# Optimization experiments

Measured on AMD Instinct MI355X. Metric: run time of the kernel, lower is better.

The kernel has to match this reference:

```python
import jax, jax.numpy as jnp
import numpy as np

B, L, H = 2, 1024, 768
DI, N, K, R = 1536, 16, 4, 48


def setup_inputs() -> dict:
    key = jax.random.key(0)
    ks = jax.random.split(key, 10)
    s = 0.02
    inp = {
        "x": jax.random.normal(ks[0], (B, L, H), jnp.float32),
        "in_up_w": jax.random.normal(ks[1], (2 * DI * 4, H), jnp.float32) * s,
        "in_down_w": jax.random.normal(ks[2], (2 * DI, 2 * DI * 4), jnp.float32) * s,
        "conv_w": jax.random.normal(ks[3], (DI, 1, K), jnp.float32) * 0.5,
        "conv_b": jnp.zeros((DI,), jnp.float32),
        "x_proj_w": jax.random.normal(ks[4], (R + 2 * N, DI), jnp.float32) * s,
        "dt_w": jax.random.normal(ks[5], (DI, R), jnp.float32) * s,
        "dt_b": jnp.full((DI,), -4.0, jnp.float32) + jax.random.normal(ks[6], (DI,), jnp.float32) * 0.1,
        "A_log": jnp.log(jnp.broadcast_to(jnp.arange(1, N + 1, dtype=jnp.float32)[None, :], (DI, N))),
        "D": jnp.ones((DI,), jnp.float32),
        "out_up_w": jax.random.normal(ks[7], (4 * DI, DI), jnp.float32) * s,
        "out_down_w": jax.random.normal(ks[8], (H, 4 * DI), jnp.float32) * s,
    }
    return inp


def reference(x, in_up_w, in_down_w, conv_w, conv_b, x_proj_w, dt_w, dt_b,
              A_log, D, out_up_w, out_down_w):
    act = jax.nn.silu
    # in_up_proj -> act -> in_down_proj  (use_bias=False)
    proj = act(x @ in_up_w.T) @ in_down_w.T          # [B, L, 2*DI]
    proj = proj.transpose(0, 2, 1)                   # [B, 2*DI, L]
    hs, gate = jnp.split(proj, 2, axis=1)            # each [B, DI, L]

    # depthwise causal conv1d (pad left K-1, truncate to L) + SiLU
    k = conv_w.shape[-1]
    c = hs.shape[1]
    y = jax.lax.conv_general_dilated(
        hs, conv_w, window_strides=(1,), padding=[(k - 1, 0)],
        feature_group_count=c, dimension_numbers=("NCH", "OIH", "NCH"))
    hs = act(y + conv_b[None, :, None])              # [B, DI, L]

    # x_proj -> split into dt / B / C
    ssm_p = jnp.einsum("bdl,kd->blk", hs, x_proj_w)  # [B, L, R+2N]
    r = dt_w.shape[1]
    n = A_log.shape[1]
    ts, Bm, Cm = jnp.split(ssm_p, [r, r + n], axis=-1)
    dt = jax.nn.softplus(ts @ dt_w.T + dt_b)         # [B, L, DI]
    dt = dt.transpose(0, 2, 1)                       # [B, DI, L]

    A = -jnp.exp(A_log)                              # [DI, N]
    dA = jnp.exp(dt[..., None] * A[None, :, None, :])        # [B, DI, L, N]
    dBu = dt[..., None] * Bm[:, None, :, :] * hs[..., None]  # [B, DI, L, N]

    def step(s, inps):
        dA_t, dBu_t, C_t = inps          # [B,DI,N], [B,DI,N], [B,N]
        s = dA_t * s + dBu_t
        return s, jnp.einsum("bdn,bn->bd", s, C_t)

    s0 = jnp.zeros((x.shape[0], c, n), x.dtype)
    _, ys = jax.lax.scan(
        step, s0,
        (dA.transpose(2, 0, 1, 3), dBu.transpose(2, 0, 1, 3), Cm.transpose(1, 0, 2)))
    yscan = ys.transpose(1, 2, 0)                    # [B, DI, L]

    yscan = yscan + hs * D[None, :, None]
    yscan = yscan * act(gate)

    # out_up_proj -> act -> out_down_proj (use_bias=False)
    out = act(yscan.transpose(0, 2, 1) @ out_up_w.T) @ out_down_w.T  # [B, L, H]
    return out
```

## Files before the change

### kernel.cpp

```cpp
#include <hip/hip_runtime.h>
#include <hip/hip_bf16.h>
#include <cstdint>

#define B_   2
#define L_   1024
#define H_   768
#define DI_  1536
#define DI2_ 3072
#define DUP_ 12288
#define DOUT_ 6144
#define N_   16
#define R_   48
#define SPW  128
#define BL_  2048
#define C_   64
#define CL_  16

typedef __bf16 bf16x8 __attribute__((ext_vector_type(8)));
typedef float  f32x4  __attribute__((ext_vector_type(4)));
typedef unsigned int u32;

__device__ __forceinline__ float silu_f(float v) {
    return v / (1.f + __expf(-v));
}

__device__ __forceinline__ void async_ld16(const void* g, void* lds) {
    __builtin_amdgcn_global_load_lds(
        (const __attribute__((address_space(1))) u32*)g,
        (__attribute__((address_space(3))) u32*)lds, 16, 0, 0);
}

__global__ void cvt_bf16(const float* __restrict__ src, __bf16* __restrict__ dst, int n)
{
    const int i = (blockIdx.x * blockDim.x + threadIdx.x) * 8;
    if (i < n) {
        const float4 a = *(const float4*)(src + i);
        const float4 b = *(const float4*)(src + i + 4);
        bf16x8 v;
        v[0] = (__bf16)a.x; v[1] = (__bf16)a.y; v[2] = (__bf16)a.z; v[3] = (__bf16)a.w;
        v[4] = (__bf16)b.x; v[5] = (__bf16)b.y; v[6] = (__bf16)b.z; v[7] = (__bf16)b.w;
        *(bf16x8*)(dst + i) = v;
    }
}

__global__ void pad_xp(const float* __restrict__ xp, __bf16* __restrict__ dst)
{
    const int i = (blockIdx.x * blockDim.x + threadIdx.x) * 8;
    const int j = i / DI_;
    bf16x8 v;
    if (j < 80) {
        const float4 a = *(const float4*)(xp + i);
        const float4 b = *(const float4*)(xp + i + 4);
        v[0] = (__bf16)a.x; v[1] = (__bf16)a.y; v[2] = (__bf16)a.z; v[3] = (__bf16)a.w;
        v[4] = (__bf16)b.x; v[5] = (__bf16)b.y; v[6] = (__bf16)b.z; v[7] = (__bf16)b.w;
    } else {
        for (int k = 0; k < 8; ++k) v[k] = (__bf16)0.f;
    }
    *(bf16x8*)(dst + i) = v;
}

__global__ void transpose_dtw(const float* __restrict__ w, float* __restrict__ wT)
{
    const int i = blockIdx.x * blockDim.x + threadIdx.x;
    const int r = i / DI_, d = i % DI_;
    wT[i] = w[(size_t)d * R_ + r];
}

template<int EPI, int ATOMIC, typename OutT>
__global__ __launch_bounds__(256) void gemm_bf16(
    const __bf16* __restrict__ A, const __bf16* __restrict__ W, OutT* __restrict__ O,
    int M, int N, int Kslice, int lda, int ldw, int ldo)
{
    constexpr int BM = 128, BN = 128, BK = 32;
    __shared__ __bf16 As[BM * BK];
    __shared__ __bf16 Bs[BN * BK];

    const int tid  = threadIdx.x;
    const int bm   = blockIdx.x * BM;
    const int bn   = blockIdx.y * BN;
    const int kbase = blockIdx.z * Kslice;

    const int wave = tid >> 6, lane = tid & 63;
    const int wm = (wave >> 1) * 64, wn = (wave & 1) * 64;
    const int quad = lane >> 4, tr = lane & 15;

    const int srow = tid >> 2;
    const int skc  = ((tid & 3) ^ ((srow >> 1) & 3)) * 8;
    const __bf16* Ag0 = A + (size_t)(bm + srow) * lda + kbase + skc;
    const __bf16* Ag1 = A + (size_t)(bm + srow + 64) * lda + kbase + skc;
    const __bf16* Wg0 = W + (size_t)(bn + srow) * ldw + kbase + skc;
    const __bf16* Wg1 = W + (size_t)(bn + srow + 64) * ldw + kbase + skc;
    __bf16* Al0 = &As[tid * 8];
    __bf16* Al1 = &As[2048 + tid * 8];
    __bf16* Bl0 = &Bs[tid * 8];
    __bf16* Bl1 = &Bs[2048 + tid * 8];

    const int fsw = (quad ^ ((tr >> 1) & 3)) * 8;
    const __bf16* arp = &As[(wm + tr) * BK + fsw];
    const __bf16* brp = &Bs[(wn + tr) * BK + fsw];

    f32x4 acc[4][4];
#pragma unroll
    for (int i = 0; i < 4; ++i)
#pragma unroll
        for (int j = 0; j < 4; ++j) acc[i][j] = (f32x4){0.f, 0.f, 0.f, 0.f};

    for (int k0 = 0; k0 < Kslice; k0 += BK) {
        __syncthreads();
        async_ld16(Ag0 + k0, Al0);
        async_ld16(Ag1 + k0, Al1);
        async_ld16(Wg0 + k0, Bl0);
        async_ld16(Wg1 + k0, Bl1);
        __syncthreads();

        bf16x8 af[4], bfv[4];
#pragma unroll
        for (int i = 0; i < 4; ++i) af[i]  = *(const bf16x8*)(arp + i * 16 * BK);
#pragma unroll
        for (int j = 0; j < 4; ++j) bfv[j] = *(const bf16x8*)(brp + j * 16 * BK);
#pragma unroll
        for (int i = 0; i < 4; ++i)
#pragma unroll
            for (int j = 0; j < 4; ++j)
                acc[i][j] = __builtin_amdgcn_mfma_f32_16x16x32_bf16(af[i], bfv[j], acc[i][j], 0, 0, 0);
    }

#pragma unroll
    for (int i = 0; i < 4; ++i) {
        const int row = bm + wm + i * 16 + quad * 4;
#pragma unroll
        for (int j = 0; j < 4; ++j) {
            const int col = bn + wn + j * 16 + tr;
            OutT* op = O + (size_t)row * ldo + col;
#pragma unroll
            for (int r = 0; r < 4; ++r) {
                float v = acc[i][j][r];
                if (EPI == 1) v = silu_f(v);
                if (ATOMIC == 1) atomicAdd((float*)(op + (size_t)r * ldo), v);
                else             op[(size_t)r * ldo] = (OutT)v;
            }
        }
    }
}

__global__ void conv_kernel(const float* __restrict__ P,
                            const float* __restrict__ cw, const float* __restrict__ cb,
                            float* __restrict__ HS, __bf16* __restrict__ HSb)
{
    const int t = blockIdx.x * blockDim.x + threadIdx.x;
    const int d = t % DI_;
    const int bl = t / DI_;
    const int l = bl % L_;
    const float4 w = *(const float4*)(cw + (size_t)d * 4);
    const float wk[4] = {w.x, w.y, w.z, w.w};
    float acc = cb[d];
#pragma unroll
    for (int k = 0; k < 4; ++k) {
        const int ls = l - 3 + k;
        if (ls >= 0)
            acc += wk[k] * P[(size_t)(bl - l + ls) * DI2_ + d];
    }
    const float h = silu_f(acc);
    HS[t]  = h;
    HSb[t] = (__bf16)h;
}

__global__ void dt_kernel(const float* __restrict__ SP, const float* __restrict__ dtwT,
                          const float* __restrict__ dtb, float* __restrict__ DT)
{
    const int t = blockIdx.x * blockDim.x + threadIdx.x;
    const int d = t % DI_;
    const int bl = t / DI_;
    const float* ts = SP + (size_t)bl * SPW;
    float s = dtb[d];
#pragma unroll
    for (int r4 = 0; r4 < R_ / 4; ++r4) {
        const float4 tv = *(const float4*)(ts + r4 * 4);
        const float* wp = dtwT + (size_t)r4 * 4 * DI_ + d;
        s += tv.x * wp[0] + tv.y * wp[DI_] + tv.z * wp[2 * DI_] + tv.w * wp[3 * DI_];
    }
    DT[t] = (s > 20.f) ? s : log1pf(__expf(s));
}

__global__ __launch_bounds__(256) void scan_pass1(
    const float* __restrict__ DT, const float* __restrict__ HS,
    const float* __restrict__ SP, const float* __restrict__ A_log,
    float* __restrict__ Aprod, float* __restrict__ Bacc)
{
    const int t = blockIdx.x * blockDim.x + threadIdx.x;
    const int d = t % DI_;
    const int y = t / DI_;
    const int c = y % C_;
    const int b = y / C_;
    float A[N_], s[N_], ap[N_];
    {
        const float4* alp = (const float4*)(A_log + (size_t)d * N_);
        const float4 a0 = alp[0], a1 = alp[1], a2 = alp[2], a3 = alp[3];
        const float av[N_] = {a0.x,a0.y,a0.z,a0.w, a1.x,a1.y,a1.z,a1.w,
                              a2.x,a2.y,a2.z,a2.w, a3.x,a3.y,a3.z,a3.w};
#pragma unroll
        for (int n = 0; n < N_; ++n) { A[n] = -__expf(av[n]); s[n] = 0.f; ap[n] = 1.f; }
    }
    for (int il = 0; il < CL_; ++il) {
        const size_t bl = (size_t)b * L_ + c * CL_ + il;
        const float dt = DT[bl * DI_ + d];
        const float hs = HS[bl * DI_ + d];
        const float4* Bp = (const float4*)(SP + bl * SPW + R_);
        const float4 b0 = Bp[0], b1 = Bp[1], b2 = Bp[2], b3 = Bp[3];
        const float Bv[N_] = {b0.x,b0.y,b0.z,b0.w, b1.x,b1.y,b1.z,b1.w,
                              b2.x,b2.y,b2.z,b2.w, b3.x,b3.y,b3.z,b3.w};
        const float dh = dt * hs;
#pragma unroll
        for (int n = 0; n < N_; ++n) {
            const float dA = __expf(dt * A[n]);
            s[n] = fmaf(dA, s[n], dh * Bv[n]);
            ap[n] *= dA;
        }
    }
    float4* Ap = (float4*)(Aprod + (size_t)t * N_);
    float4* Bc = (float4*)(Bacc  + (size_t)t * N_);
    Ap[0] = make_float4(ap[0], ap[1], ap[2], ap[3]);
    Ap[1] = make_float4(ap[4], ap[5], ap[6], ap[7]);
    Ap[2] = make_float4(ap[8], ap[9], ap[10], ap[11]);
    Ap[3] = make_float4(ap[12], ap[13], ap[14], ap[15]);
    Bc[0] = make_float4(s[0], s[1], s[2], s[3]);
    Bc[1] = make_float4(s[4], s[5], s[6], s[7]);
    Bc[2] = make_float4(s[8], s[9], s[10], s[11]);
    Bc[3] = make_float4(s[12], s[13], s[14], s[15]);
}

__global__ __launch_bounds__(256) void scan_pass2(
    const float* __restrict__ Aprod, const float* __restrict__ Bacc,
    float* __restrict__ Sinit)
{
    const int t = blockIdx.x * blockDim.x + threadIdx.x;
    const int n = t & (N_ - 1);
    const int d = (t >> 4) % DI_;
    const int b = (t >> 4) / DI_;
    float s = 0.f;
    for (int c = 0; c < C_; ++c) {
        const size_t idx = (((size_t)b * C_ + c) * DI_ + d) * N_ + n;
        Sinit[idx] = s;
        s = fmaf(Aprod[idx], s, Bacc[idx]);
    }
}

__global__ __launch_bounds__(256) void scan_pass3(
    const float* __restrict__ DT, const float* __restrict__ HS,
    const float* __restrict__ SP, const float* __restrict__ P,
    const float* __restrict__ A_log, const float* __restrict__ Dv,
    const float* __restrict__ Sinit, __bf16* __restrict__ Y)
{
    const int t = blockIdx.x * blockDim.x + threadIdx.x;
    const int d = t % DI_;
    const int y = t / DI_;
    const int c = y % C_;
    const int b = y / C_;
    float A[N_], s[N_];
    {
        const float4* alp = (const float4*)(A_log + (size_t)d * N_);
        const float4 a0 = alp[0], a1 = alp[1], a2 = alp[2], a3 = alp[3];
        const float av[N_] = {a0.x,a0.y,a0.z,a0.w, a1.x,a1.y,a1.z,a1.w,
                              a2.x,a2.y,a2.z,a2.w, a3.x,a3.y,a3.z,a3.w};
#pragma unroll
        for (int n = 0; n < N_; ++n) A[n] = -__expf(av[n]);
    }
    {
        const float4* sp = (const float4*)(Sinit + (size_t)t * N_);
        const float4 s0 = sp[0], s1 = sp[1], s2 = sp[2], s3 = sp[3];
        s[0]=s0.x; s[1]=s0.y; s[2]=s0.z; s[3]=s0.w;
        s[4]=s1.x; s[5]=s1.y; s[6]=s1.z; s[7]=s1.w;
        s[8]=s2.x; s[9]=s2.y; s[10]=s2.z; s[11]=s2.w;
        s[12]=s3.x; s[13]=s3.y; s[14]=s3.z; s[15]=s3.w;
    }
    const float Dd = Dv[d];
    for (int il = 0; il < CL_; ++il) {
        const size_t bl = (size_t)b * L_ + c * CL_ + il;
        const float dt = DT[bl * DI_ + d];
        const float hs = HS[bl * DI_ + d];
        const float4* Bp = (const float4*)(SP + bl * SPW + R_);
        const float4 b0 = Bp[0], b1 = Bp[1], b2 = Bp[2], b3 = Bp[3];
        const float4 c0 = Bp[4], c1 = Bp[5], c2 = Bp[6], c3 = Bp[7];
        const float Bv[N_] = {b0.x,b0.y,b0.z,b0.w, b1.x,b1.y,b1.z,b1.w,
                              b2.x,b2.y,b2.z,b2.w, b3.x,b3.y,b3.z,b3.w};
        const float Cv[N_] = {c0.x,c0.y,c0.z,c0.w, c1.x,c1.y,c1.z,c1.w,
                              c2.x,c2.y,c2.z,c2.w, c3.x,c3.y,c3.z,c3.w};
        const float dh = dt * hs;
        float acc = 0.f;
#pragma unroll
        for (int n = 0; n < N_; ++n) {
            const float dA = __expf(dt * A[n]);
            s[n] = fmaf(dA, s[n], dh * Bv[n]);
            acc = fmaf(s[n], Cv[n], acc);
        }
        const float g = P[bl * DI2_ + DI_ + d];
        Y[bl * DI_ + d] = (__bf16)((acc + hs * Dd) * silu_f(g));
    }
}

extern "C" void kernel_launch(void* const* d_in, const int* in_sizes, int n_in,
                              void* d_out, int out_size, void* d_ws, size_t ws_size,
                              hipStream_t stream) {
    const float* x        = (const float*)d_in[0];
    const float* w_up     = (const float*)d_in[1];
    const float* w_down   = (const float*)d_in[2];
    const float* conv_w   = (const float*)d_in[3];
    const float* conv_b   = (const float*)d_in[4];
    const float* x_proj_w = (const float*)d_in[5];
    const float* dt_w     = (const float*)d_in[6];
    const float* dt_b     = (const float*)d_in[7];
    const float* A_log    = (const float*)d_in[8];
    const float* Dvec     = (const float*)d_in[9];
    const float* w_oup    = (const float*)d_in[10];
    const float* w_odown  = (const float*)d_in[11];
    float* out = (float*)d_out;

    char* base = (char*)d_ws;
    __bf16* x_b      = (__bf16*)base;
    __bf16* wup_b    = (__bf16*)(base + 3145728);
    float*  P        = (float*)base;
    char* r2 = base + 25165824;
    __bf16* wdown_b  = (__bf16*)r2;
    __bf16* HSb      = (__bf16*)r2;
    float*  SPb      = (float*)(r2 + 6291456);
    float*  DTb      = (float*)(r2 + 7340032);
    __bf16* Yb       = (__bf16*)(r2 + 19922944);
    __bf16* XPpad    = (__bf16*)(r2 + 26214400);
    float*  dtwT     = (float*)(r2 + 26607616);
    __bf16* woup_b   = (__bf16*)(r2 + 26902528);
    __bf16* wodown_b = (__bf16*)(r2 + 45776896);
    char* r3 = r2 + 75497472;
    __bf16* U1b      = (__bf16*)r3;
    __bf16* U2b      = (__bf16*)r3;
    float*  Aprod    = (float*)r3;
    float*  Bacc     = (float*)(r3 + 12582912);
    float*  Sinit    = (float*)(r3 + 25165824);
    char* r4 = r3 + 50331648;
    float*  HS       = (float*)r4;

    cvt_bf16<<<(BL_ * H_) / 2048, 256, 0, stream>>>(x, x_b, BL_ * H_);
    cvt_bf16<<<(DUP_ * H_) / 2048, 256, 0, stream>>>(w_up, wup_b, DUP_ * H_);
    cvt_bf16<<<(DI2_ * DUP_) / 2048, 256, 0, stream>>>(w_down, wdown_b, DI2_ * DUP_);

    gemm_bf16<1, 0, __bf16><<<dim3(16, 96, 1), 256, 0, stream>>>(
        x_b, wup_b, U1b, BL_, DUP_, H_, H_, H_, DUP_);

    hipMemsetAsync(P, 0, (size_t)BL_ * DI2_ * 4, stream);
    gemm_bf16<0, 1, float><<<dim3(16, 24, 4), 256, 0, stream>>>(
        U1b, wdown_b, P, BL_, DI2_, DUP_ / 4, DUP_, DUP_, DI2_);

    pad_xp<<<(128 * DI_) / 2048, 256, 0, stream>>>(x_proj_w, XPpad);
    transpose_dtw<<<(R_ * DI_) / 256, 256, 0, stream>>>(dt_w, dtwT);
    cvt_bf16<<<(DOUT_ * DI_) / 2048, 256, 0, stream>>>(w_oup, woup_b, DOUT_ * DI_);
    cvt_bf16<<<(H_ * DOUT_) / 2048, 256, 0, stream>>>(w_odown, wodown_b, H_ * DOUT_);

    conv_kernel<<<(BL_ * DI_) / 256, 256, 0, stream>>>(P, conv_w, conv_b, HS, HSb);

    hipMemsetAsync(SPb, 0, (size_t)BL_ * SPW * 4, stream);
    gemm_bf16<0, 1, float><<<dim3(16, 1, 4), 256, 0, stream>>>(
        HSb, XPpad, SPb, BL_, SPW, DI_ / 4, DI_, DI_, SPW);

    dt_kernel<<<(BL_ * DI_) / 256, 256, 0, stream>>>(SPb, dtwT, dt_b, DTb);

    scan_pass1<<<(B_ * C_ * DI_) / 256, 256, 0, stream>>>(DTb, HS, SPb, A_log, Aprod, Bacc);
    scan_pass2<<<(B_ * DI_ * N_) / 256, 256, 0, stream>>>(Aprod, Bacc, Sinit);
    scan_pass3<<<(B_ * C_ * DI_) / 256, 256, 0, stream>>>(
        DTb, HS, SPb, P, A_log, Dvec, Sinit, Yb);

    gemm_bf16<1, 0, __bf16><<<dim3(16, 48, 1), 256, 0, stream>>>(
        Yb, woup_b, U2b, BL_, DOUT_, DI_, DI_, DI_, DOUT_);

    hipMemsetAsync(out, 0, (size_t)BL_ * H_ * 4, stream);
    gemm_bf16<0, 1, float><<<dim3(16, 6, 8), 256, 0, stream>>>(
        U2b, wodown_b, out, BL_, H_, DOUT_ / 8, DOUT_, DOUT_, H_);
}
```

Measured before the change: 856.5 us.

## Add 256x256-tile 512-thread GEMM with 4-stage async pipeline for two projections

Introduces a new GEMM kernel with 256x256 output tiles, 8 waves, a 4-slot LDS ring filled by async global-to-LDS loads, XOR-swizzled shared layout, split A/B staging interleaved with MFMA phases, s_setprio around the MFMA blocks, and a grouped block-index swizzle for L2 locality. It replaces the in_down split-K GEMM (now split 8 ways) and the out_up GEMM. The larger tiles raise arithmetic intensity and cut global/LDS traffic per FLOP. In exchange it uses 128 KB of dynamic LDS and many accumulator registers, which limits occupancy, and the grids become much smaller, which risks underfilling the CUs.

```diff
diff --git a/kernel.cpp b/kernel.cpp
--- a/kernel.cpp
+++ b/kernel.cpp
@@ -135,6 +135,137 @@
 #pragma unroll
             for (int r = 0; r < 4; ++r) {
                 float v = acc[i][j][r];
+                if (EPI == 1) v = silu_f(v);
+                if (ATOMIC == 1) atomicAdd((float*)(op + (size_t)r * ldo), v);
+                else             op[(size_t)r * ldo] = (OutT)v;
+            }
+        }
+    }
+}
+
+template<int EPI, int ATOMIC, typename OutT>
+__global__ __launch_bounds__(512, 2) void gemm256(
+    const __bf16* __restrict__ A, const __bf16* __restrict__ W, OutT* __restrict__ O,
+    int M, int N, int Kslice, int lda, int ldw, int ldo)
+{
+    extern __shared__ __bf16 S[];
+    __bf16* AS = S;
+    __bf16* BS = S + 32768;
+
+    const int tid = threadIdx.x;
+
+    const int nxy  = gridDim.x * gridDim.y;
+    const int flat = blockIdx.x + gridDim.x * blockIdx.y;
+    const int q    = nxy >> 3;
+    const int swz  = (flat & 7) * q + (flat >> 3);
+    const int bm   = (swz % gridDim.x) * 256;
+    const int bn   = (swz / gridDim.x) * 256;
+    const int kbase = blockIdx.z * Kslice;
+    const int NT    = Kslice >> 5;
+
+    const int srow = tid >> 2;
+    const int skc  = ((tid & 3) ^ ((tid >> 3) & 3)) * 8;
+    const __bf16* Ag = A + (size_t)(bm + srow) * lda + kbase + skc;
+    const __bf16* Wg = W + (size_t)(bn + srow) * ldw + kbase + skc;
+    const size_t ldA128 = (size_t)128 * lda;
+    const size_t ldW128 = (size_t)128 * ldw;
+    __bf16* Asl = AS + tid * 8;
+    __bf16* Bsl = BS + tid * 8;
+
+    auto stageA = [&](int t) {
+        const int sl = (t & 3) * 8192;
+        const __bf16* g = Ag + t * 32;
+        async_ld16(g,          Asl + sl);
+        async_ld16(g + ldA128, Asl + sl + 4096);
+    };
+    auto stageB = [&](int t) {
+        const int sl = (t & 3) * 8192;
+        const __bf16* g = Wg + t * 32;
+        async_ld16(g,          Bsl + sl);
+        async_ld16(g + ldW128, Bsl + sl + 4096);
+    };
+
+    const int wv = tid >> 6, lane = tid & 63;
+    const int wr = wv >> 2, wc = wv & 3;
+    const int quad = lane >> 4, tr = lane & 15;
+    const int fsw = (quad ^ ((tr >> 1) & 3)) * 8;
+    const __bf16* arp = AS + (wr * 128 + tr) * 32 + fsw;
+    const __bf16* brp = BS + (wc * 64 + tr) * 32 + fsw;
+
+    f32x4 acc[8][4];
+#pragma unroll
+    for (int i = 0; i < 8; ++i)
+#pragma unroll
+        for (int j = 0; j < 4; ++j) acc[i][j] = (f32x4){0.f, 0.f, 0.f, 0.f};
+
+    const int npre = NT < 3 ? NT : 3;
+    for (int t = 0; t < npre; ++t) { stageA(t); stageB(t); }
+    __builtin_amdgcn_sched_barrier(0);
+    if (NT > 3) asm volatile("s_waitcnt vmcnt(8)" ::: "memory");
+    else        asm volatile("s_waitcnt vmcnt(0)" ::: "memory");
+    __builtin_amdgcn_s_barrier();
+    __builtin_amdgcn_sched_barrier(0);
+
+    for (int g = 0; g < NT; ++g) {
+        const int sl = (g & 3) * 8192;
+        const __bf16* ar = arp + sl;
+        const __bf16* br = brp + sl;
+        bf16x8 a0[4], a1[4], bv[4];
+
+#pragma unroll
+        for (int f = 0; f < 4; ++f) a0[f] = *(const bf16x8*)(ar + f * 16 * 32);
+#pragma unroll
+        for (int j = 0; j < 4; ++j) bv[j] = *(const bf16x8*)(br + j * 16 * 32);
+        if (g + 3 < NT) stageA(g + 3);
+        __builtin_amdgcn_sched_barrier(0);
+        __builtin_amdgcn_s_barrier();
+        __builtin_amdgcn_sched_barrier(0);
+        __builtin_amdgcn_s_setprio(1);
+#pragma unroll
+        for (int f = 0; f < 4; ++f)
+#pragma unroll
+            for (int j = 0; j < 4; ++j)
+                acc[f][j] = __builtin_amdgcn_mfma_f32_16x16x32_bf16(a0[f], bv[j], acc[f][j], 0, 0, 0);
+        __builtin_amdgcn_s_setprio(0);
+        __builtin_amdgcn_sched_barrier(0);
+        __builtin_amdgcn_s_barrier();
+        __builtin_amdgcn_sched_barrier(0);
+
+#pragma unroll
+        for (int f = 0; f < 4; ++f) a1[f] = *(const bf16x8*)(ar + (64 + f * 16) * 32);
+        if (g + 3 < NT) stageB(g + 3);
+        __builtin_amdgcn_sched_barrier(0);
+        __builtin_amdgcn_s_barrier();
+        __builtin_amdgcn_sched_barrier(0);
+        __builtin_amdgcn_s_setprio(1);
+#pragma unroll
+        for (int f = 0; f < 4; ++f)
+#pragma unroll
+            for (int j = 0; j < 4; ++j)
+                acc[4 + f][j] = __builtin_amdgcn_mfma_f32_16x16x32_bf16(a1[f], bv[j], acc[4 + f][j], 0, 0, 0);
+        __builtin_amdgcn_s_setprio(0);
+        __builtin_amdgcn_sched_barrier(0);
+
+        const int rem = NT - 1 - g;
+        if (rem >= 3)      asm volatile("s_waitcnt vmcnt(8)" ::: "memory");
+        else if (rem == 2) asm volatile("s_waitcnt vmcnt(4)" ::: "memory");
+        else if (rem == 1) asm volatile("s_waitcnt vmcnt(0)" ::: "memory");
+        if (rem > 0) {
+            __builtin_amdgcn_s_barrier();
+            __builtin_amdgcn_sched_barrier(0);
+        }
+    }
+
+#pragma unroll
+    for (int fi = 0; fi < 8; ++fi) {
+        const int row = bm + wr * 128 + fi * 16 + quad * 4;
+#pragma unroll
+        for (int fj = 0; fj < 4; ++fj) {
+            const int col = bn + wc * 64 + fj * 16 + tr;
+            OutT* op = O + (size_t)row * ldo + col;
+#pragma unroll
+            for (int r = 0; r < 4; ++r) {
+                float v = acc[fi][fj][r];
                 if (EPI == 1) v = silu_f(v);
                 if (ATOMIC == 1) atomicAdd((float*)(op + (size_t)r * ldo), v);
                 else             op[(size_t)r * ldo] = (OutT)v;
@@ -314,6 +445,15 @@
     const float* w_oup    = (const float*)d_in[10];
     const float* w_odown  = (const float*)d_in[11];
     float* out = (float*)d_out;
+
+    static bool attr_done = []() {
+        hipFuncSetAttribute(reinterpret_cast<const void*>(&gemm256<0, 1, float>),
+                            hipFuncAttributeMaxDynamicSharedMemorySize, 131072);
+        hipFuncSetAttribute(reinterpret_cast<const void*>(&gemm256<1, 0, __bf16>),
+                            hipFuncAttributeMaxDynamicSharedMemorySize, 131072);
+        return true;
+    }();
+    (void)attr_done;
 
     char* base = (char*)d_ws;
     __bf16* x_b      = (__bf16*)base;
@@ -346,8 +486,8 @@
         x_b, wup_b, U1b, BL_, DUP_, H_, H_, H_, DUP_);
 
     hipMemsetAsync(P, 0, (size_t)BL_ * DI2_ * 4, stream);
-    gemm_bf16<0, 1, float><<<dim3(16, 24, 4), 256, 0, stream>>>(
-        U1b, wdown_b, P, BL_, DI2_, DUP_ / 4, DUP_, DUP_, DI2_);
+    gemm256<0, 1, float><<<dim3(8, 12, 8), 512, 131072, stream>>>(
+        U1b, wdown_b, P, BL_, DI2_, DUP_ / 8, DUP_, DUP_, DI2_);
 
     pad_xp<<<(128 * DI_) / 2048, 256, 0, stream>>>(x_proj_w, XPpad);
     transpose_dtw<<<(R_ * DI_) / 256, 256, 0, stream>>>(dt_w, dtwT);
@@ -367,7 +507,7 @@
     scan_pass3<<<(B_ * C_ * DI_) / 256, 256, 0, stream>>>(
         DTb, HS, SPb, P, A_log, Dvec, Sinit, Yb);
 
-    gemm_bf16<1, 0, __bf16><<<dim3(16, 48, 1), 256, 0, stream>>>(
+    gemm256<1, 0, __bf16><<<dim3(8, 24, 1), 512, 131072, stream>>>(
         Yb, woup_b, U2b, BL_, DOUT_, DI_, DI_, DI_, DOUT_);
 
     hipMemsetAsync(out, 0, (size_t)BL_ * H_ * 4, stream);
```

Measured after the change: 889.5 us. 3.9% more time.
